# Kernel optimization log

Hardware: AMD Instinct MI355X
Metric: run time of the kernel (lower is better)

Reference implementation:

```python
import jax, jax.numpy as jnp
import numpy as np

B, N, C_IN = 16, 1024, 24
EMB, OUT, HEADS = 64, 12, 2
EMBED_SIZE = 12
HID = EMB // 2
INFLATION = 25.0


def setup_inputs() -> dict:
    rng = np.random.RandomState(0)
    # binary adjacency: ~16 random out-neighbors per node + self loops
    A = np.zeros((N, N), np.float32)
    A[np.repeat(np.arange(N), 16), rng.randint(0, N, N * 16)] = 1.0
    A[np.arange(N), np.arange(N)] = 1.0
    src, dst = np.nonzero(A)  # row-major order == torch.nonzero order
    E = src.shape[0]
    key = jax.random.key(0)
    ks = iter(jax.random.split(key, 40))

    def nrm(shape, s=0.05):
        return jax.random.normal(next(ks), shape, jnp.float32) * s

    return dict(
        x=nrm((B, N, C_IN), 1.0),
        adj=jnp.asarray(A),
        edge_index=jnp.stack([jnp.asarray(src, jnp.int32), jnp.asarray(dst, jnp.int32)]),
        edge_weight=jax.random.uniform(next(ks), (E,), jnp.float32, 0.1, 1.0),
        Wq=nrm((C_IN, C_IN)), bq=jnp.zeros((C_IN,), jnp.float32),
        Wk=nrm((C_IN, C_IN)), bk=jnp.zeros((C_IN,), jnp.float32),
        Wd=nrm((2, 2, C_IN, EMB)), bd=jnp.zeros((EMB,), jnp.float32),
        c1w0=nrm((64, C_IN, 2)), c1b0=jnp.zeros((64,), jnp.float32),
        c2w0=nrm((64, 64, 2)), c2b0=jnp.zeros((64,), jnp.float32),
        dw0=nrm((64, C_IN, 1)), db0=jnp.zeros((64,), jnp.float32),
        c1w1=nrm((EMB, 64, 2)), c1b1=jnp.zeros((EMB,), jnp.float32),
        c2w1=nrm((EMB, EMB, 2)), c2b1=jnp.zeros((EMB,), jnp.float32),
        We=nrm((EMBED_SIZE, 2 * EMB)), be=jnp.zeros((EMBED_SIZE,), jnp.float32),
        Wih=nrm((3 * HID, EMBED_SIZE)), Whh=nrm((3 * HID, HID)),
        bih=jnp.zeros((3 * HID,), jnp.float32), bhh=jnp.zeros((3 * HID,), jnp.float32),
        Wdec=nrm((OUT, HID)), bdec=jnp.zeros((OUT,), jnp.float32),
    )


def _causal_conv(x, w, b, dil):
    # torch: pad both sides by p then Chomp1d(p) on the right == left-pad only
    p = (w.shape[-1] - 1) * dil
    y = jax.lax.conv_general_dilated(x, w, (1,), [(p, 0)], rhs_dilation=(dil,),
                                     dimension_numbers=('NCH', 'OIH', 'NCH'))
    return y + b[None, :, None]


def _forward(x, adj, edge_index, edge_weight, Wq, bq, Wk, bk, Wd, bd,
             c1w0, c1b0, c2w0, c2b0, dw0, db0, c1w1, c1b1, c2w1, c2b1,
             We, be, Wih, Whh, bih, bhh, Wdec, bdec):
    src, dst = edge_index[0], edge_index[1]
    hd = C_IN // HEADS
    # --- MultiheadAttention: only averaged attn weights are used ---
    q = (x @ Wq.T + bq).reshape(B, N, HEADS, hd).transpose(0, 2, 1, 3)
    k = (x @ Wk.T + bk).reshape(B, N, HEADS, hd).transpose(0, 2, 1, 3)
    attn = jax.nn.softmax(jnp.einsum('bhqd,bhkd->bhqk', q, k) / float(np.sqrt(hd)), axis=-1)
    attn = attn.mean(axis=1)  # (B,N,N) average over heads (torch default)
    mean_w = jnp.mean(adj[None] * attn, axis=0)  # (N,N)
    # torch.nonzero(Mean_weight) == adjacency support (softmax > 0), row-major
    att_score = mean_w[src, dst]  # (E,)
    ew = INFLATION * edge_weight * att_score
    # --- DConv K=2 (torch_geometric_temporal): weighted degrees, norm*x_j messages ---
    deg_out = jnp.zeros((N,), x.dtype).at[src].add(ew)
    deg_in = jnp.zeros((N,), x.dtype).at[dst].add(ew)
    inv_out = 1.0 / deg_out
    inv_in = 1.0 / deg_in
    t1o = jnp.zeros_like(x).at[:, dst].add(x[:, src] * inv_out[src][None, :, None])
    t1i = jnp.zeros_like(x).at[:, src].add(x[:, dst] * inv_in[dst][None, :, None])
    spatial = x @ Wd[0, 0] + x @ Wd[1, 0] + t1o @ Wd[0, 1] + t1i @ Wd[1, 1] + bd
    spatial = jax.nn.relu(spatial)  # (B,N,EMB)
    # --- TCN over the node axis (x.permute(0,2,1)), dropout=identity (eval) ---
    h = x.transpose(0, 2, 1)  # (B,C,N)
    o = jax.nn.relu(_causal_conv(h, c1w0, c1b0, 1))
    o = jax.nn.relu(_causal_conv(o, c2w0, c2b0, 1))
    h = jax.nn.relu(o + _causal_conv(h, dw0, db0, 1))  # block0: downsample 1x1
    o = jax.nn.relu(_causal_conv(h, c1w1, c1b1, 2))
    o = jax.nn.relu(_causal_conv(o, c2w1, c2b1, 2))
    h = jax.nn.relu(o + h)  # block1: identity residual
    temporal = jax.nn.relu(h.transpose(0, 2, 1))  # (B,N,EMB)
    # --- fuse + embed + GRU decoder ---
    emb = jnp.concatenate([temporal, spatial], axis=-1) @ We.T + be  # (B,N,12)
    xp = emb @ Wih.T + bih  # (B,N,3H) precomputed input projections

    def step(hprev, xt):
        gh = hprev @ Whh.T + bhh
        xr, xz, xn = jnp.split(xt, 3, axis=-1)
        hr, hz, hn = jnp.split(gh, 3, axis=-1)
        r = jax.nn.sigmoid(xr + hr)
        z = jax.nn.sigmoid(xz + hz)
        n = jnp.tanh(xn + r * hn)
        hnew = (1.0 - z) * n + z * hprev
        return hnew, hnew

    _, hs = jax.lax.scan(step, jnp.zeros((B, HID), x.dtype), xp.transpose(1, 0, 2))
    hfeat = jax.nn.relu(hs.transpose(1, 0, 2))  # (B,N,HID)
    return hfeat @ Wdec.T + bdec  # (B,N,OUT)


def reference(x, adj, edge_index, edge_weight, Wq, bq, Wk, bk, Wd, bd,
              c1w0, c1b0, c2w0, c2b0, dw0, db0, c1w1, c1b1, c2w1, c2b1,
              We, be, Wih, Whh, bih, bhh, Wdec, bdec):
    return _forward(x, adj, edge_index, edge_weight, Wq, bq, Wk, bk, Wd, bd,
                    c1w0, c1b0, c2w0, c2b0, dw0, db0, c1w1, c1b1, c2w1, c2b1,
                    We, be, Wih, Whh, bih, bhh, Wdec, bdec)
```

## Files before the change

### kernel.cpp

```cpp
#include <hip/hip_runtime.h>
#include <hip/hip_bf16.h>

#define B_ 16
#define N_ 1024
#define CIN 24
#define EMB_ 64
#define HID_ 32
#define OUT_ 12
#define BH_ 32
#define RSQRT12 0.28867513459481287f
#define L2E 1.4426950408889634f

typedef unsigned uvec2 __attribute__((ext_vector_type(2)));
typedef float f2 __attribute__((ext_vector_type(2)));

#define OFF_Q      0
#define OFF_K      393216
#define OFF_M      786432
#define OFF_ZI     819200
#define OFF_DEG    851968
#define OFF_INT    854016
#define OFF_TEMP   2689024
#define OFF_WFT    3737600
#define OFF_BF     3749888
#define OFF_XP     3750016

__global__ __launch_bounds__(1024) void qk_prep_kernel(
    const float* __restrict__ x, const float* __restrict__ Wq, const float* __restrict__ bq,
    const float* __restrict__ Wk, const float* __restrict__ bk,
    float* __restrict__ q, float* __restrict__ k,
    const int* __restrict__ ei, int E,
    float* __restrict__ deg, int* __restrict__ rp, int* __restrict__ cp,
    int* __restrict__ eids,
    const float* __restrict__ We, const float* __restrict__ be,
    const float* __restrict__ Wih, const float* __restrict__ bih,
    float* __restrict__ WfT, float* __restrict__ bf) {
  __shared__ int cntL[1024];
  __shared__ int sL[1024];
  __shared__ int offL[1024];
  int tid = threadIdx.x;
  if (blockIdx.x == 0) {
    deg[tid] = 0.f; deg[N_ + tid] = 0.f;
    cntL[tid] = 0;
    { int lo = 0, hi2 = E;
      while (lo < hi2) { int mid = (lo + hi2) >> 1; if (ei[mid] < tid) lo = mid + 1; else hi2 = mid; }
      rp[tid] = lo; }
    if (tid == 0) rp[N_] = E;
    __syncthreads();
    for (int e = tid; e < E; e += 1024) atomicAdd(&cntL[ei[E + e]], 1);
    __syncthreads();
    int my = cntL[tid];
    sL[tid] = my;
    __syncthreads();
    for (int d = 1; d < 1024; d <<= 1) {
      int v = (tid >= d) ? sL[tid - d] : 0;
      __syncthreads();
      sL[tid] += v;
      __syncthreads();
    }
    int excl = sL[tid] - my;
    cp[tid] = excl;
    offL[tid] = excl;
    if (tid == 1023) cp[1024] = sL[tid];
    __syncthreads();
    for (int e = tid; e < E; e += 1024) {
      int p = atomicAdd(&offL[ei[E + e]], 1);
      eids[p] = e;
    }
    for (int i = tid; i < 128 * 96; i += 1024) {
      int o = i % 96, c = i / 96;
      float acc = 0.f;
#pragma unroll
      for (int e = 0; e < 12; e++) acc += Wih[o * 12 + e] * We[e * 128 + c];
      WfT[c * 96 + o] = acc * ((o < 64) ? L2E : 2.f * L2E);
    }
    if (tid < 96) {
      float acc = bih[tid];
#pragma unroll
      for (int e = 0; e < 12; e++) acc += Wih[tid * 12 + e] * be[e];
      bf[tid] = acc * ((tid < 64) ? L2E : 2.f * L2E);
    }
  } else {
    int t = (blockIdx.x - 1) * 1024 + tid;
    int bi = t / CIN, c = t % CIN;
    int b = bi >> 10, i = bi & (N_ - 1);
    const float* xr = x + bi * CIN;
    float aq = bq[c], ak = bk[c];
#pragma unroll
    for (int d = 0; d < CIN; d++) {
      float xv = xr[d];
      aq += xv * Wq[c * CIN + d];
      ak += xv * Wk[c * CIN + d];
    }
    int h = c / 12, cc = c - h * 12;
    int qi = ((b * 2 + h) * N_ + i) * 12 + cc;
    q[qi] = aq;
    k[qi] = ak;
  }
}

#define TW 72
__global__ __launch_bounds__(512) void lse_tcn_kernel(
    const float* __restrict__ q, const float* __restrict__ k,
    float* __restrict__ mrow, float* __restrict__ zinv,
    const float* __restrict__ x,
    const float* __restrict__ c1w0, const float* __restrict__ c1b0,
    const float* __restrict__ c2w0, const float* __restrict__ c2b0,
    const float* __restrict__ dw0, const float* __restrict__ db0,
    const float* __restrict__ c1w1, const float* __restrict__ c1b1,
    const float* __restrict__ c2w1, const float* __restrict__ c2b1,
    float* __restrict__ temporal) {
  __shared__ __align__(16) char smem[53248];
  int tid = threadIdx.x;
  if (blockIdx.x < 512) {
    float* ks = (float*)smem;
    float (*pm)[64] = (float(*)[64])(smem + 49152);
    float (*pz)[64] = (float(*)[64])(smem + 51200);
    int bh = blockIdx.x >> 4;
    int rg = blockIdx.x & 15;
    const float4* k4 = (const float4*)(k + bh * N_ * 12);
    float4* ks4 = (float4*)ks;
    for (int i = tid; i < N_ * 3; i += 512) ks4[i] = k4[i];
    int wave = tid >> 6, lane = tid & 63;
    int row = rg * 64 + lane;
    float qr[12];
    const float* qp = q + (bh * N_ + row) * 12;
#pragma unroll
    for (int c = 0; c < 12; c++) qr[c] = qp[c];
    __syncthreads();
    float mloc = -1e30f, zloc = 0.f;
    for (int j = wave * 128; j < wave * 128 + 128; j++) {
      const float* kj = ks + j * 12;
      float s = 0.f;
#pragma unroll
      for (int c = 0; c < 12; c++) s += qr[c] * kj[c];
      s *= RSQRT12;
      float mn = fmaxf(mloc, s);
      zloc = zloc * __expf(mloc - mn) + __expf(s - mn);
      mloc = mn;
    }
    pm[wave][lane] = mloc;
    pz[wave][lane] = zloc;
    __syncthreads();
    if (tid < 64) {
      float M = pm[0][tid];
#pragma unroll
      for (int w2 = 1; w2 < 8; w2++) M = fmaxf(M, pm[w2][tid]);
      float Z = 0.f;
#pragma unroll
      for (int w2 = 0; w2 < 8; w2++) Z += pz[w2][tid] * __expf(pm[w2][tid] - M);
      mrow[bh * N_ + rg * 64 + tid] = M;
      zinv[bh * N_ + rg * 64 + tid] = 1.f / Z;
    }
  } else {
    float* xs   = (float*)smem;
    float* bufA = xs + CIN * TW;
    float* bufB = bufA + 64 * TW;
    int tb = blockIdx.x - 512;
    int b = tb >> 4;
    int t0 = (tb & 15) << 6;
    int co = tid & 63, g = tid >> 6;
    for (int i = tid; i < CIN * TW; i += 512) {
      int ln = i / CIN, c = i % CIN;
      int n = t0 - 6 + ln;
      xs[c * TW + ln] = (n >= 0 && n < N_) ? x[(b * N_ + n) * CIN + c] : 0.f;
    }
    __syncthreads();
    {
      int lbase = 1 + g * 9;
      float acc[9];
      float bias = c1b0[co];
#pragma unroll
      for (int kk = 0; kk < 9; kk++) acc[kk] = bias;
      const float* wrow = c1w0 + co * 48;
      for (int ci = 0; ci < 24; ci++) {
        float w0 = wrow[ci * 2], w1 = wrow[ci * 2 + 1];
        const float* in = xs + ci * TW + lbase;
        float prev = in[-1];
#pragma unroll
        for (int kk = 0; kk < 9; kk++) { float cur = in[kk]; acc[kk] += w0 * prev + w1 * cur; prev = cur; }
      }
#pragma unroll
      for (int kk = 0; kk < 9; kk++) {
        int ln = lbase + kk;
        if (ln < TW) { int n = t0 - 6 + ln; bufB[co * TW + ln] = (n >= 0) ? fmaxf(acc[kk], 0.f) : 0.f; }
      }
    }
    __syncthreads();
    {
      int lbase = 2 + g * 9;
      float acc[9], ds[9];
      float bias = c2b0[co], dbias = db0[co];
#pragma unroll
      for (int kk = 0; kk < 9; kk++) { acc[kk] = bias; ds[kk] = dbias; }
      const float* wrow = c2w0 + co * 128;
      for (int ci = 0; ci < 64; ci++) {
        float w0 = wrow[ci * 2], w1 = wrow[ci * 2 + 1];
        const float* in = bufB + ci * TW + lbase;
        float prev = in[-1];
#pragma unroll
        for (int kk = 0; kk < 9; kk++) { float cur = in[kk]; acc[kk] += w0 * prev + w1 * cur; prev = cur; }
      }
      const float* wd = dw0 + co * 24;
      for (int ci = 0; ci < 24; ci++) {
        float wv = wd[ci];
        const float* in = xs + ci * TW + lbase;
#pragma unroll
        for (int kk = 0; kk < 9; kk++) ds[kk] += wv * in[kk];
      }
#pragma unroll
      for (int kk = 0; kk < 9; kk++) {
        int ln = lbase + kk;
        if (ln < TW) {
          int n = t0 - 6 + ln;
          float v = fmaxf(fmaxf(acc[kk], 0.f) + ds[kk], 0.f);
          bufA[co * TW + ln] = (n >= 0) ? v : 0.f;
        }
      }
    }
    __syncthreads();
    {
      int lbase = 4 + g * 9;
      float acc[9];
      float bias = c1b1[co];
#pragma unroll
      for (int kk = 0; kk < 9; kk++) acc[kk] = bias;
      const float* wrow = c1w1 + co * 128;
      for (int ci = 0; ci < 64; ci++) {
        float w0 = wrow[ci * 2], w1 = wrow[ci * 2 + 1];
        const float* in = bufA + ci * TW + lbase;
        float p2 = in[-2], p1 = in[-1];
#pragma unroll
        for (int kk = 0; kk < 9; kk++) { float cur = in[kk]; acc[kk] += w0 * p2 + w1 * cur; p2 = p1; p1 = cur; }
      }
#pragma unroll
      for (int kk = 0; kk < 9; kk++) {
        int ln = lbase + kk;
        if (ln < TW) { int n = t0 - 6 + ln; bufB[co * TW + ln] = (n >= 0) ? fmaxf(acc[kk], 0.f) : 0.f; }
      }
    }
    __syncthreads();
    {
      int lbase = 6 + g * 8;
      float acc[8];
      float bias = c2b1[co];
#pragma unroll
      for (int kk = 0; kk < 8; kk++) acc[kk] = bias;
      const float* wrow = c2w1 + co * 128;
      for (int ci = 0; ci < 64; ci++) {
        float w0 = wrow[ci * 2], w1 = wrow[ci * 2 + 1];
        const float* in = bufB + ci * TW + lbase;
        float p2 = in[-2], p1 = in[-1];
#pragma unroll
        for (int kk = 0; kk < 8; kk++) { float cur = in[kk]; acc[kk] += w0 * p2 + w1 * cur; p2 = p1; p1 = cur; }
      }
#pragma unroll
      for (int kk = 0; kk < 8; kk++) {
        int ln = lbase + kk;
        float v = fmaxf(fmaxf(acc[kk], 0.f) + bufA[co * TW + ln], 0.f);
        temporal[(b * N_ + t0 + ln - 6) * 64 + co] = v;
      }
    }
  }
}

__global__ __launch_bounds__(256) void edge_stats_kernel(
    const float* __restrict__ q, const float* __restrict__ k,
    const float* __restrict__ mrow, const float* __restrict__ zinv,
    const int* __restrict__ ei, const float* __restrict__ ewt, int E,
    float* __restrict__ deg) {
  int t = blockIdx.x * 256 + threadIdx.x;
  int e = t >> 5, bh = t & 31;
  if (e >= E) return;
  int src = ei[e], dst = ei[E + e];
  const float4* qp = (const float4*)(q + (bh * N_ + src) * 12);
  const float4* kp = (const float4*)(k + (bh * N_ + dst) * 12);
  float s = 0.f;
#pragma unroll
  for (int c4 = 0; c4 < 3; c4++) {
    float4 qv = qp[c4], kv = kp[c4];
    s += qv.x * kv.x + qv.y * kv.y + qv.z * kv.z + qv.w * kv.w;
  }
  s *= RSQRT12;
  float a = __expf(s - mrow[bh * N_ + src]) * zinv[bh * N_ + src];
  a += __shfl_xor(a, 16);
  a += __shfl_xor(a, 8);
  a += __shfl_xor(a, 4);
  a += __shfl_xor(a, 2);
  a += __shfl_xor(a, 1);
  if (bh == 0) {
    float w = 25.f * ewt[e] * (a * (1.f / 32.f));
    atomicAdd(&deg[src], w);
    atomicAdd(&deg[N_ + dst], w);
  }
}

__global__ __launch_bounds__(384) void gather_io_kernel(
    const float* __restrict__ x, const int* __restrict__ ei, int E,
    const int* __restrict__ rp, const int* __restrict__ cp, const int* __restrict__ eids,
    const float* __restrict__ deg,
    float* __restrict__ t1i, float* __restrict__ t1o) {
  __shared__ int nb[96];
  __shared__ float wv[96];
  bool isOut = blockIdx.x >= N_;
  int node = isOut ? (blockIdx.x - N_) : blockIdx.x;
  int e0 = isOut ? cp[node] : rp[node];
  int e1 = isOut ? cp[node + 1] : rp[node + 1];
  int tid = threadIdx.x;
  int b = tid / 24, c = tid % 24;
  float acc = 0.f;
  for (int base = e0; base < e1; base += 96) {
    int m = min(96, e1 - base);
    if (tid < m) {
      if (isOut) {
        int e = eids[base + tid];
        int sn = ei[e];
        nb[tid] = sn;
        wv[tid] = __builtin_amdgcn_rcpf(deg[sn]);
      } else {
        int d = ei[E + base + tid];
        nb[tid] = d;
        wv[tid] = __builtin_amdgcn_rcpf(deg[N_ + d]);
      }
    }
    __syncthreads();
    for (int t = 0; t < m; t++) acc += x[(b * N_ + nb[t]) * CIN + c] * wv[t];
    __syncthreads();
  }
  float* dst = isOut ? t1o : t1i;
  dst[(b * N_ + node) * CIN + c] = acc;
}

__global__ __launch_bounds__(384) void spatxp_kernel(
    const float* __restrict__ x, const float* __restrict__ t1o, const float* __restrict__ t1i,
    const float* __restrict__ Wd, const float* __restrict__ bd,
    const float* __restrict__ temporal,
    const float* __restrict__ WfT, const float* __restrict__ bf,
    float* __restrict__ xp) {
  __shared__ float tmp_s[64 * 64];
  __shared__ float spat_s[64 * 64];
  int b = blockIdx.x >> 4;
  int n0 = (blockIdx.x & 15) << 6;
  int tid = threadIdx.x;
  {
    const float4* t4 = (const float4*)(temporal + (size_t)(b * N_ + n0) * 64);
    float4* d4 = (float4*)tmp_s;
    for (int i = tid; i < 1024; i += 384) d4[i] = t4[i];
  }
  for (int idx = tid; idx < 4096; idx += 384) {
    int nl = idx >> 6, o = idx & 63;
    int bi = (b * N_ + n0 + nl);
    const float* xr = x + bi * CIN;
    const float* ar = t1o + bi * CIN;
    const float* br = t1i + bi * CIN;
    float acc = bd[o];
#pragma unroll
    for (int d = 0; d < CIN; d++) {
      acc += xr[d] * (Wd[d * 64 + o] + Wd[3072 + d * 64 + o]);
      acc += ar[d] * Wd[1536 + d * 64 + o];
      acc += br[d] * Wd[4608 + d * 64 + o];
    }
    spat_s[nl * 64 + o] = fmaxf(acc, 0.f);
  }
  __syncthreads();
  {
    int g = tid / 96, o = tid - g * 96;
    float acc[16];
#pragma unroll
    for (int kk = 0; kk < 16; kk++) acc[kk] = bf[o];
    const float* tr = tmp_s + g * 16 * 64;
    const float* sr = spat_s + g * 16 * 64;
    for (int c = 0; c < 64; c++) {
      float w1 = WfT[c * 96 + o];
      float w2 = WfT[(64 + c) * 96 + o];
#pragma unroll
      for (int kk = 0; kk < 16; kk++) {
        acc[kk] = fmaf(tr[kk * 64 + c], w1, fmaf(sr[kk * 64 + c], w2, acc[kk]));
      }
    }
#pragma unroll
    for (int kk = 0; kk < 16; kk++)
      xp[(size_t)(b * N_ + n0 + g * 16 + kk) * 96 + o] = acc[kk];
  }
}

#define CHUNK 64
__global__ __launch_bounds__(256) void gru_kernel(
    const float* __restrict__ xp, const float* __restrict__ Whh,
    const float* __restrict__ bhh, const float* __restrict__ Wdec,
    const float* __restrict__ bdec, float* __restrict__ out) {
  __shared__ float xbuf[2][CHUNK * 96];
  __shared__ float hbuf[2][CHUNK * 36];
  __shared__ float wdec_s[12 * 36];
  __shared__ float bdec_s[12];
  int b = blockIdx.x, tid = threadIdx.x;
  int wave = tid >> 6, j = tid & 63, jl = j & 31, hi = j >> 5;
  const float* xpb = xp + (size_t)b * N_ * 96;
  {
    const float4* s4 = (const float4*)xpb;
    float4* d4 = (float4*)xbuf[0];
    for (int i = tid; i < CHUNK * 24; i += 256) d4[i] = s4[i];
    if (tid < 12) bdec_s[tid] = bdec[tid];
    for (int i = tid; i < 384; i += 256) wdec_s[(i >> 5) * 36 + (i & 31)] = Wdec[i];
  }
  f2 wA2[16], wB2[16];
  float bA = 0.f, bB = 0.f, hloc = 0.f;
  int xoff = hi ? (32 + jl) : jl;
  if (wave == 0) {
    int rowA = hi ? (32 + jl) : jl;
#pragma unroll
    for (int i = 0; i < 16; i++) {
      wA2[i] = f2{L2E * Whh[rowA * 32 + 2 * i], L2E * Whh[rowA * 32 + 2 * i + 1]};
      wB2[i] = f2{2.f * L2E * Whh[(64 + jl) * 32 + 2 * i], 2.f * L2E * Whh[(64 + jl) * 32 + 2 * i + 1]};
    }
    bA = L2E * bhh[rowA];
    bB = 2.f * L2E * bhh[64 + jl];
  }
  float4 hv4[8];
#pragma unroll
  for (int i = 0; i < 8; i++) hv4[i] = float4{0.f, 0.f, 0.f, 0.f};
  __syncthreads();
  for (int c = 0; c < 16; c++) {
    if (wave == 0) {
      const float* buf = xbuf[c & 1];
      float* hb = hbuf[c & 1];
      float xga = buf[xoff] + bA;
      float xnv = buf[64 + jl];
      for (int ln = 0; ln < CHUNK; ln++) {
        float nxga = 0.f, nxnv = 0.f;
        if (ln + 1 < CHUNK) {
          nxga = buf[(ln + 1) * 96 + xoff] + bA;
          nxnv = buf[(ln + 1) * 96 + 64 + jl];
        }
        f2 aA = f2{xga, 0.f};
        f2 aB = f2{bB, 0.f};
#pragma unroll
        for (int i = 0; i < 8; i++) {
          f2 h01 = f2{hv4[i].x, hv4[i].y};
          f2 h23 = f2{hv4[i].z, hv4[i].w};
          aA = __builtin_elementwise_fma(wA2[2 * i], h01, aA);
          aB = __builtin_elementwise_fma(wB2[2 * i], h01, aB);
          aA = __builtin_elementwise_fma(wA2[2 * i + 1], h23, aA);
          aB = __builtin_elementwise_fma(wB2[2 * i + 1], h23, aB);
        }
        float gA = aA.x + aA.y;
        float gB = aB.x + aB.y;
        float sg = __builtin_amdgcn_rcpf(1.f + exp2f(-gA));
#if __has_builtin(__builtin_amdgcn_permlane32_swap)
        uvec2 sw = __builtin_amdgcn_permlane32_swap(__float_as_uint(sg), __float_as_uint(sg), false, false);
        float zv = __uint_as_float(sw.y);
#else
        float zv = __shfl_xor(sg, 32);
#endif
        float pre = fmaf(sg, gB, xnv);
        float t = exp2f(pre);
        float nn = fmaf(-2.f, __builtin_amdgcn_rcpf(t + 1.f), 1.f);
        hloc = fmaf(zv, hloc - nn, nn);
        if (j < 32) hb[ln * 36 + jl] = hloc;
        const float4* hrow = (const float4*)(hb + ln * 36);
#pragma unroll
        for (int i = 0; i < 8; i++) hv4[i] = hrow[i];
        xga = nxga; xnv = nxnv;
      }
    } else {
      int t64 = tid - 64;
      if (c + 1 < 16) {
        const float4* s4 = (const float4*)(xpb + (size_t)(c + 1) * CHUNK * 96);
        float4* d4 = (float4*)xbuf[(c + 1) & 1];
        for (int i = t64; i < CHUNK * 24; i += 192) d4[i] = s4[i];
      }
      if (c > 0) {
        const float* hb = hbuf[(c - 1) & 1];
        int n0b = (c - 1) * CHUNK;
#pragma unroll
        for (int qq = 0; qq < 4; qq++) {
          int idx = qq * 192 + t64;
          int nl = idx / 12, o = idx - nl * 12;
          const float4* h4 = (const float4*)(hb + nl * 36);
          const float4* w4 = (const float4*)(wdec_s + o * 36);
          float acc = bdec_s[o];
#pragma unroll
          for (int i = 0; i < 8; i++) {
            float4 hv = h4[i], wv = w4[i];
            acc += fmaxf(hv.x, 0.f) * wv.x + fmaxf(hv.y, 0.f) * wv.y +
                   fmaxf(hv.z, 0.f) * wv.z + fmaxf(hv.w, 0.f) * wv.w;
          }
          out[(size_t)(b * N_ + n0b + nl) * 12 + o] = acc;
        }
      }
    }
    __syncthreads();
  }
  {
    const float* hb = hbuf[1];
    int n0b = 15 * CHUNK;
#pragma unroll
    for (int qq = 0; qq < 3; qq++) {
      int idx = qq * 256 + tid;
      int nl = idx / 12, o = idx - nl * 12;
      const float4* h4 = (const float4*)(hb + nl * 36);
      const float4* w4 = (const float4*)(wdec_s + o * 36);
      float acc = bdec_s[o];
#pragma unroll
      for (int i = 0; i < 8; i++) {
        float4 hv = h4[i], wv = w4[i];
        acc += fmaxf(hv.x, 0.f) * wv.x + fmaxf(hv.y, 0.f) * wv.y +
               fmaxf(hv.z, 0.f) * wv.z + fmaxf(hv.w, 0.f) * wv.w;
      }
      out[(size_t)(b * N_ + n0b + nl) * 12 + o] = acc;
    }
  }
}

extern "C" void kernel_launch(void* const* d_in, const int* in_sizes, int n_in,
                              void* d_out, int out_size, void* d_ws, size_t ws_size,
                              hipStream_t stream) {
  const float* x    = (const float*)d_in[0];
  const int*   ei   = (const int*)d_in[2];
  const float* ewt  = (const float*)d_in[3];
  const float* Wq   = (const float*)d_in[4];
  const float* bq   = (const float*)d_in[5];
  const float* Wk   = (const float*)d_in[6];
  const float* bk   = (const float*)d_in[7];
  const float* Wd   = (const float*)d_in[8];
  const float* bd   = (const float*)d_in[9];
  const float* c1w0 = (const float*)d_in[10];
  const float* c1b0 = (const float*)d_in[11];
  const float* c2w0 = (const float*)d_in[12];
  const float* c2b0 = (const float*)d_in[13];
  const float* dw0  = (const float*)d_in[14];
  const float* db0  = (const float*)d_in[15];
  const float* c1w1 = (const float*)d_in[16];
  const float* c1b1 = (const float*)d_in[17];
  const float* c2w1 = (const float*)d_in[18];
  const float* c2b1 = (const float*)d_in[19];
  const float* We   = (const float*)d_in[20];
  const float* be   = (const float*)d_in[21];
  const float* Wih  = (const float*)d_in[22];
  const float* Whh  = (const float*)d_in[23];
  const float* bih  = (const float*)d_in[24];
  const float* bhh  = (const float*)d_in[25];
  const float* Wdec = (const float*)d_in[26];
  const float* bdec = (const float*)d_in[27];
  float* out = (float*)d_out;
  float* w = (float*)d_ws;
  const int E = in_sizes[2] / 2;

  float* q    = w + OFF_Q;
  float* k    = w + OFF_K;
  float* mrow = w + OFF_M;
  float* zinv = w + OFF_ZI;
  float* deg  = w + OFF_DEG;
  float* t1o  = w + OFF_Q;
  float* t1i  = w + OFF_K;
  float* temp = w + OFF_TEMP;
  float* WfT  = w + OFF_WFT;
  float* bf   = w + OFF_BF;
  float* xp   = w + OFF_XP;
  int* ib   = (int*)(w + OFF_INT);
  int* rp   = ib;
  int* cp   = ib + 1028;
  int* eids = ib + 2056;

  qk_prep_kernel<<<385, 1024, 0, stream>>>(x, Wq, bq, Wk, bk, q, k,
                                           ei, E, deg, rp, cp, eids,
                                           We, be, Wih, bih, WfT, bf);
  lse_tcn_kernel<<<768, 512, 0, stream>>>(q, k, mrow, zinv, x,
                                          c1w0, c1b0, c2w0, c2b0, dw0, db0,
                                          c1w1, c1b1, c2w1, c2b1, temp);
  edge_stats_kernel<<<(E * 32 + 255) / 256, 256, 0, stream>>>(q, k, mrow, zinv, ei, ewt, E, deg);
  gather_io_kernel<<<2 * N_, 384, 0, stream>>>(x, ei, E, rp, cp, eids, deg, t1i, t1o);
  spatxp_kernel<<<B_ * 16, 384, 0, stream>>>(x, t1o, t1i, Wd, bd, temp, WfT, bf, xp);
  gru_kernel<<<B_, 256, 0, stream>>>(xp, Whh, bhh, Wdec, bdec, out);
}
```

Baseline: 379.1 us.

## Store Q/K and row stats node-major, stage spatial inputs in LDS, split GRU FMA chains

Q, row max and inverse normaliser are now stored node-major, interleaved across batch-head. A second node-major copy of K is also written. This lets the edge-statistics kernel, where 32 consecutive threads share one edge, read contiguous memory. The logsumexp loop reads K from LDS as float4 instead of scalar loads. The spatial projection kernel stages its x, t1o and t1i tiles in shared memory before use. The GRU recurrence splits its dot-product accumulators into four independent chains to shorten the FMA dependency on the serial critical path, at the cost of an extra K write and more LDS.

```diff
diff --git a/kernel.cpp b/kernel.cpp
--- a/kernel.cpp
+++ b/kernel.cpp
@@ -14,21 +14,22 @@
 typedef unsigned uvec2 __attribute__((ext_vector_type(2)));
 typedef float f2 __attribute__((ext_vector_type(2)));
 
-#define OFF_Q      0
-#define OFF_K      393216
-#define OFF_M      786432
-#define OFF_ZI     819200
-#define OFF_DEG    851968
-#define OFF_INT    854016
-#define OFF_TEMP   2689024
-#define OFF_WFT    3737600
-#define OFF_BF     3749888
-#define OFF_XP     3750016
+#define OFF_Q2     0
+#define OFF_K1     393216
+#define OFF_K2     786432
+#define OFF_M      1179648
+#define OFF_ZI     1212416
+#define OFF_DEG    1245184
+#define OFF_INT    1247232
+#define OFF_TEMP   1271296
+#define OFF_WFT    2319872
+#define OFF_BF     2332160
+#define OFF_XP     2332288
 
 __global__ __launch_bounds__(1024) void qk_prep_kernel(
     const float* __restrict__ x, const float* __restrict__ Wq, const float* __restrict__ bq,
     const float* __restrict__ Wk, const float* __restrict__ bk,
-    float* __restrict__ q, float* __restrict__ k,
+    float* __restrict__ q2, float* __restrict__ k1, float* __restrict__ k2,
     const int* __restrict__ ei, int E,
     float* __restrict__ deg, int* __restrict__ rp, int* __restrict__ cp,
     int* __restrict__ eids,
@@ -93,16 +94,17 @@
       ak += xv * Wk[c * CIN + d];
     }
     int h = c / 12, cc = c - h * 12;
-    int qi = ((b * 2 + h) * N_ + i) * 12 + cc;
-    q[qi] = aq;
-    k[qi] = ak;
+    int bh2 = b * 2 + h;
+    q2[(i * 32 + bh2) * 12 + cc] = aq;
+    k1[(bh2 * N_ + i) * 12 + cc] = ak;
+    k2[(i * 32 + bh2) * 12 + cc] = ak;
   }
 }
 
 #define TW 72
 __global__ __launch_bounds__(512) void lse_tcn_kernel(
-    const float* __restrict__ q, const float* __restrict__ k,
-    float* __restrict__ mrow, float* __restrict__ zinv,
+    const float* __restrict__ q2, const float* __restrict__ k1,
+    float* __restrict__ mrow2, float* __restrict__ zinv2,
     const float* __restrict__ x,
     const float* __restrict__ c1w0, const float* __restrict__ c1b0,
     const float* __restrict__ c2w0, const float* __restrict__ c2b0,
@@ -118,22 +120,23 @@
     float (*pz)[64] = (float(*)[64])(smem + 51200);
     int bh = blockIdx.x >> 4;
     int rg = blockIdx.x & 15;
-    const float4* k4 = (const float4*)(k + bh * N_ * 12);
+    const float4* k4 = (const float4*)(k1 + bh * N_ * 12);
     float4* ks4 = (float4*)ks;
     for (int i = tid; i < N_ * 3; i += 512) ks4[i] = k4[i];
     int wave = tid >> 6, lane = tid & 63;
     int row = rg * 64 + lane;
     float qr[12];
-    const float* qp = q + (bh * N_ + row) * 12;
+    const float* qp = q2 + ((size_t)row * 32 + bh) * 12;
 #pragma unroll
     for (int c = 0; c < 12; c++) qr[c] = qp[c];
     __syncthreads();
+    const float4* ksr = (const float4*)ks;
     float mloc = -1e30f, zloc = 0.f;
     for (int j = wave * 128; j < wave * 128 + 128; j++) {
-      const float* kj = ks + j * 12;
-      float s = 0.f;
-#pragma unroll
-      for (int c = 0; c < 12; c++) s += qr[c] * kj[c];
+      float4 k0 = ksr[j * 3], k1v = ksr[j * 3 + 1], k2v = ksr[j * 3 + 2];
+      float s = qr[0] * k0.x + qr[1] * k0.y + qr[2] * k0.z + qr[3] * k0.w
+              + qr[4] * k1v.x + qr[5] * k1v.y + qr[6] * k1v.z + qr[7] * k1v.w
+              + qr[8] * k2v.x + qr[9] * k2v.y + qr[10] * k2v.z + qr[11] * k2v.w;
       s *= RSQRT12;
       float mn = fmaxf(mloc, s);
       zloc = zloc * __expf(mloc - mn) + __expf(s - mn);
@@ -149,8 +152,9 @@
       float Z = 0.f;
 #pragma unroll
       for (int w2 = 0; w2 < 8; w2++) Z += pz[w2][tid] * __expf(pm[w2][tid] - M);
-      mrow[bh * N_ + rg * 64 + tid] = M;
-      zinv[bh * N_ + rg * 64 + tid] = 1.f / Z;
+      int node = rg * 64 + tid;
+      mrow2[node * 32 + bh] = M;
+      zinv2[node * 32 + bh] = 1.f / Z;
     }
   } else {
     float* xs   = (float*)smem;
@@ -265,16 +269,16 @@
 }
 
 __global__ __launch_bounds__(256) void edge_stats_kernel(
-    const float* __restrict__ q, const float* __restrict__ k,
-    const float* __restrict__ mrow, const float* __restrict__ zinv,
+    const float* __restrict__ q2, const float* __restrict__ k2,
+    const float* __restrict__ mrow2, const float* __restrict__ zinv2,
     const int* __restrict__ ei, const float* __restrict__ ewt, int E,
     float* __restrict__ deg) {
   int t = blockIdx.x * 256 + threadIdx.x;
   int e = t >> 5, bh = t & 31;
   if (e >= E) return;
   int src = ei[e], dst = ei[E + e];
-  const float4* qp = (const float4*)(q + (bh * N_ + src) * 12);
-  const float4* kp = (const float4*)(k + (bh * N_ + dst) * 12);
+  const float4* qp = (const float4*)(q2 + ((size_t)src * 32 + bh) * 12);
+  const float4* kp = (const float4*)(k2 + ((size_t)dst * 32 + bh) * 12);
   float s = 0.f;
 #pragma unroll
   for (int c4 = 0; c4 < 3; c4++) {
@@ -282,7 +286,7 @@
     s += qv.x * kv.x + qv.y * kv.y + qv.z * kv.z + qv.w * kv.w;
   }
   s *= RSQRT12;
-  float a = __expf(s - mrow[bh * N_ + src]) * zinv[bh * N_ + src];
+  float a = __expf(s - mrow2[src * 32 + bh]) * zinv2[src * 32 + bh];
   a += __shfl_xor(a, 16);
   a += __shfl_xor(a, 8);
   a += __shfl_xor(a, 4);
@@ -339,6 +343,7 @@
     float* __restrict__ xp) {
   __shared__ float tmp_s[64 * 64];
   __shared__ float spat_s[64 * 64];
+  __shared__ float xs3[3 * 64 * 24];
   int b = blockIdx.x >> 4;
   int n0 = (blockIdx.x & 15) << 6;
   int tid = threadIdx.x;
@@ -346,13 +351,21 @@
     const float4* t4 = (const float4*)(temporal + (size_t)(b * N_ + n0) * 64);
     float4* d4 = (float4*)tmp_s;
     for (int i = tid; i < 1024; i += 384) d4[i] = t4[i];
-  }
+    size_t base = (size_t)(b * N_ + n0) * 24;
+    const float4* xsrc = (const float4*)(x + base);
+    const float4* asrc = (const float4*)(t1o + base);
+    const float4* bsrc = (const float4*)(t1i + base);
+    float4* xd = (float4*)xs3;
+    xd[tid] = xsrc[tid];
+    xd[384 + tid] = asrc[tid];
+    xd[768 + tid] = bsrc[tid];
+  }
+  __syncthreads();
   for (int idx = tid; idx < 4096; idx += 384) {
     int nl = idx >> 6, o = idx & 63;
-    int bi = (b * N_ + n0 + nl);
-    const float* xr = x + bi * CIN;
-    const float* ar = t1o + bi * CIN;
-    const float* br = t1i + bi * CIN;
+    const float* xr = xs3 + nl * 24;
+    const float* ar = xs3 + 1536 + nl * 24;
+    const float* br = xs3 + 3072 + nl * 24;
     float acc = bd[o];
 #pragma unroll
     for (int d = 0; d < CIN; d++) {
@@ -432,19 +445,27 @@
           nxga = buf[(ln + 1) * 96 + xoff] + bA;
           nxnv = buf[(ln + 1) * 96 + 64 + jl];
         }
-        f2 aA = f2{xga, 0.f};
-        f2 aB = f2{bB, 0.f};
-#pragma unroll
-        for (int i = 0; i < 8; i++) {
-          f2 h01 = f2{hv4[i].x, hv4[i].y};
-          f2 h23 = f2{hv4[i].z, hv4[i].w};
-          aA = __builtin_elementwise_fma(wA2[2 * i], h01, aA);
-          aB = __builtin_elementwise_fma(wB2[2 * i], h01, aB);
-          aA = __builtin_elementwise_fma(wA2[2 * i + 1], h23, aA);
-          aB = __builtin_elementwise_fma(wB2[2 * i + 1], h23, aB);
+        f2 aA0 = f2{xga, 0.f}, aA1 = f2{0.f, 0.f}, aA2 = f2{0.f, 0.f}, aA3 = f2{0.f, 0.f};
+        f2 aB0 = f2{bB, 0.f},  aB1 = f2{0.f, 0.f}, aB2 = f2{0.f, 0.f}, aB3 = f2{0.f, 0.f};
+#pragma unroll
+        for (int i = 0; i < 8; i += 2) {
+          f2 h01a = f2{hv4[i].x, hv4[i].y};
+          f2 h23a = f2{hv4[i].z, hv4[i].w};
+          f2 h01b = f2{hv4[i + 1].x, hv4[i + 1].y};
+          f2 h23b = f2{hv4[i + 1].z, hv4[i + 1].w};
+          aA0 = __builtin_elementwise_fma(wA2[2 * i], h01a, aA0);
+          aA1 = __builtin_elementwise_fma(wA2[2 * i + 1], h23a, aA1);
+          aA2 = __builtin_elementwise_fma(wA2[2 * i + 2], h01b, aA2);
+          aA3 = __builtin_elementwise_fma(wA2[2 * i + 3], h23b, aA3);
+          aB0 = __builtin_elementwise_fma(wB2[2 * i], h01a, aB0);
+          aB1 = __builtin_elementwise_fma(wB2[2 * i + 1], h23a, aB1);
+          aB2 = __builtin_elementwise_fma(wB2[2 * i + 2], h01b, aB2);
+          aB3 = __builtin_elementwise_fma(wB2[2 * i + 3], h23b, aB3);
         }
-        float gA = aA.x + aA.y;
-        float gB = aB.x + aB.y;
+        f2 rA = (aA0 + aA1) + (aA2 + aA3);
+        f2 rB = (aB0 + aB1) + (aB2 + aB3);
+        float gA = rA.x + rA.y;
+        float gB = rB.x + rB.y;
         float sg = __builtin_amdgcn_rcpf(1.f + exp2f(-gA));
 #if __has_builtin(__builtin_amdgcn_permlane32_swap)
         uvec2 sw = __builtin_amdgcn_permlane32_swap(__float_as_uint(sg), __float_as_uint(sg), false, false);
@@ -546,29 +567,30 @@
   float* w = (float*)d_ws;
   const int E = in_sizes[2] / 2;
 
-  float* q    = w + OFF_Q;
-  float* k    = w + OFF_K;
-  float* mrow = w + OFF_M;
-  float* zinv = w + OFF_ZI;
-  float* deg  = w + OFF_DEG;
-  float* t1o  = w + OFF_Q;
-  float* t1i  = w + OFF_K;
-  float* temp = w + OFF_TEMP;
-  float* WfT  = w + OFF_WFT;
-  float* bf   = w + OFF_BF;
-  float* xp   = w + OFF_XP;
+  float* q2    = w + OFF_Q2;
+  float* k1    = w + OFF_K1;
+  float* k2    = w + OFF_K2;
+  float* mrow2 = w + OFF_M;
+  float* zinv2 = w + OFF_ZI;
+  float* deg   = w + OFF_DEG;
+  float* t1o   = w + OFF_Q2;
+  float* t1i   = w + OFF_K1;
+  float* temp  = w + OFF_TEMP;
+  float* WfT   = w + OFF_WFT;
+  float* bf    = w + OFF_BF;
+  float* xp    = w + OFF_XP;
   int* ib   = (int*)(w + OFF_INT);
   int* rp   = ib;
   int* cp   = ib + 1028;
   int* eids = ib + 2056;
 
-  qk_prep_kernel<<<385, 1024, 0, stream>>>(x, Wq, bq, Wk, bk, q, k,
+  qk_prep_kernel<<<385, 1024, 0, stream>>>(x, Wq, bq, Wk, bk, q2, k1, k2,
                                            ei, E, deg, rp, cp, eids,
                                            We, be, Wih, bih, WfT, bf);
-  lse_tcn_kernel<<<768, 512, 0, stream>>>(q, k, mrow, zinv, x,
+  lse_tcn_kernel<<<768, 512, 0, stream>>>(q2, k1, mrow2, zinv2, x,
                                           c1w0, c1b0, c2w0, c2b0, dw0, db0,
                                           c1w1, c1b1, c2w1, c2b1, temp);
-  edge_stats_kernel<<<(E * 32 + 255) / 256, 256, 0, stream>>>(q, k, mrow, zinv, ei, ewt, E, deg);
+  edge_stats_kernel<<<(E * 32 + 255) / 256, 256, 0, stream>>>(q2, k2, mrow2, zinv2, ei, ewt, E, deg);
   gather_io_kernel<<<2 * N_, 384, 0, stream>>>(x, ei, E, rp, cp, eids, deg, t1i, t1o);
   spatxp_kernel<<<B_ * 16, 384, 0, stream>>>(x, t1o, t1i, Wd, bd, temp, WfT, bf, xp);
   gru_kernel<<<B_, 256, 0, stream>>>(xp, Whh, bhh, Wdec, bdec, out);
```

Result: no change. 380.6 us (+0.4%).
